# Performance work log

Measured on AMD Instinct MI355X. Metric: run time of the kernel, lower is better.

The kernel has to match this reference:

```python
import jax, jax.numpy as jnp
import numpy as np

SEQ, B, D_IN, D_TRAJ, D_LSTM = 640, 40, 8, 32, 64
NH, DH = 4, 48  # n_head, att_out
EMB = NH * DH  # 192


def setup_inputs() -> dict:
    key = jax.random.key(0)
    ks = jax.random.split(key, 16)
    g = lambda k, shape: (jax.random.normal(k, shape, dtype=jnp.float32) * 0.05)
    z = lambda n: jnp.zeros((n,), jnp.float32)
    return {
        "hist": jax.random.normal(ks[0], (128, 5, 40, D_IN), dtype=jnp.float32),
        "adj": jnp.zeros((B, B), dtype=jnp.int32),  # unused (use_spatial=False)
        "W1": g(ks[1], (D_TRAJ, D_IN)), "b1": z(D_TRAJ),
        "W_ih": g(ks[2], (4 * D_LSTM, D_TRAJ)), "W_hh": g(ks[3], (4 * D_LSTM, D_LSTM)),
        "b_ih": z(4 * D_LSTM), "b_hh": z(4 * D_LSTM),
        "Wq": g(ks[4], (EMB, D_LSTM)), "bq": z(EMB),
        "Wk": g(ks[5], (EMB, D_LSTM)), "bk": z(EMB),
        "Wv": g(ks[6], (EMB, D_LSTM)), "bv": z(EMB),
        "Wa": g(ks[7], (D_LSTM, EMB)), "ba": z(D_LSTM),
        "Wg": g(ks[8], (D_LSTM, EMB)), "bg": z(D_LSTM),
        "gamma": jnp.ones((D_LSTM,), jnp.float32), "beta": z(D_LSTM),
    }


def reference(hist, adj, W1, b1, W_ih, W_hh, b_ih, b_hh,
              Wq, bq, Wk, bk, Wv, bv, Wa, ba, Wg, bg, gamma, beta):
    # trajectory embedding + ELU
    x = jax.nn.elu(jnp.einsum('...f,hf->...h', hist, W1) + b1)
    x = x.reshape(SEQ, B, D_TRAJ)  # hardcoded (128*5, 40, 32) in the module

    # single-layer LSTM (torch gate order i, f, g, o), seq-first
    def step(carry, xt):
        h, c = carry
        gates = xt @ W_ih.T + h @ W_hh.T + b_ih + b_hh
        i, f, g_, o = jnp.split(gates, 4, axis=-1)
        c = jax.nn.sigmoid(f) * c + jax.nn.sigmoid(i) * jnp.tanh(g_)
        h = jax.nn.sigmoid(o) * jnp.tanh(c)
        return (h, c), h

    h0 = jnp.zeros((B, D_LSTM), x.dtype)
    (_, _), seq = jax.lax.scan(step, (h0, h0), x)  # (640, 40, 64)

    # multi-head attention over the 40-agent axis, per time step
    def heads(W, b):
        y = seq @ W.T + b  # (640, 40, 192)
        return y.reshape(SEQ, B, NH, DH).transpose(2, 0, 1, 3)  # (4, 640, 40, 48)

    q, k, v = heads(Wq, bq), heads(Wk, bk), heads(Wv, bv)
    a = jax.nn.softmax(jnp.einsum('hnqd,hnkd->hnqk', q, k) / 8.0, axis=-1)  # /sqrt(64)
    o = jnp.einsum('hnqk,hnkd->hnqd', a, v)  # (4, 640, 40, 48)
    o = o.transpose(1, 2, 0, 3).reshape(SEQ, B, EMB)  # recombine heads -> (640, 40, 192)

    # GLU (dropout rate = 0)
    tv = (o @ Wa.T + ba) * jax.nn.sigmoid(o @ Wg.T + bg)  # (640, 40, 64)

    # Add & LayerNorm (residual with LSTM output)
    y = seq + tv
    mu = y.mean(-1, keepdims=True)
    var = ((y - mu) ** 2).mean(-1, keepdims=True)
    return (y - mu) / jnp.sqrt(var + 1e-5) * gamma + beta
```

## Files before the change

### kernel.cpp

```cpp
#include <hip/hip_runtime.h>

#define SEQ 640
#define BATCH 40
#define D_IN 8
#define D_TRAJ 32
#define D_LSTM 64
#define G4 256
#define NH 4
#define DH 48
#define EMB 192

typedef float v2f __attribute__((ext_vector_type(2)));
typedef float v4f __attribute__((ext_vector_type(4)));
typedef _Float16 h2t __attribute__((ext_vector_type(2)));

__device__ __forceinline__ float sigmoid_f(float x) {
    float e = __expf(-x);
    return __builtin_amdgcn_rcpf(1.f + e);
}
__device__ __forceinline__ float tanh_f(float x) {
    float e = __expf(2.f * x);
    return 1.f - 2.f * __builtin_amdgcn_rcpf(e + 1.f);
}

__global__ void __launch_bounds__(256) k_embed(
    const float* __restrict__ hist, const float* __restrict__ W1,
    const float* __restrict__ b1, const float* __restrict__ W_ih,
    const float* __restrict__ b_ih, const float* __restrict__ b_hh,
    float* __restrict__ gates_x)
{
    __shared__ float sh_hist[BATCH * D_IN];
    __shared__ __align__(16) float sh_traj[BATCH * D_TRAJ];
    const int t = blockIdx.x, tid = threadIdx.x;

    for (int i = tid; i < BATCH * D_IN; i += 256)
        sh_hist[i] = hist[t * BATCH * D_IN + i];
    __syncthreads();

    for (int idx = tid; idx < BATCH * D_TRAJ; idx += 256) {
        int b = idx >> 5, h = idx & 31;
        float acc = b1[h];
        #pragma unroll
        for (int f = 0; f < D_IN; ++f)
            acc += sh_hist[b * D_IN + f] * W1[h * D_IN + f];
        sh_traj[idx] = acc > 0.f ? acc : (__expf(acc) - 1.f);
    }
    __syncthreads();

    float w[D_TRAJ];
    {
        const v4f* wv = (const v4f*)(W_ih + tid * D_TRAJ);
        #pragma unroll
        for (int u = 0; u < 8; ++u) {
            v4f x = wv[u];
            w[4*u] = x.x; w[4*u+1] = x.y; w[4*u+2] = x.z; w[4*u+3] = x.w;
        }
    }
    const float bias = b_ih[tid] + b_hh[tid];
    const int j = tid & 63, g = tid >> 6;

    for (int b = 0; b < BATCH; ++b) {
        const v4f* tp = (const v4f*)&sh_traj[b * D_TRAJ];
        float acc = bias;
        #pragma unroll
        for (int u = 0; u < 8; ++u) {
            v4f tv = tp[u];
            acc += tv.x * w[4*u];
            acc += tv.y * w[4*u+1];
            acc += tv.z * w[4*u+2];
            acc += tv.w * w[4*u+3];
        }
        gates_x[(((size_t)b * 4 + g) * SEQ + t) * 64 + j] = acc;
    }
}

__global__ void __launch_bounds__(256, 1) k_lstm(
    const float* __restrict__ gates_x, const float* __restrict__ W_hh,
    float* __restrict__ seq_out)
{
    const int b = blockIdx.x;
    const int tid = threadIdx.x;
    const int g = tid >> 6;
    const int j = tid & 63;

    __shared__ float sg[2][4][64];

    h2t w2[32];
    {
        const float* Wrow = W_hh + (g * 64 + j) * D_LSTM;
        #pragma unroll
        for (int m = 0; m < 32; ++m)
            w2[m] = (h2t){(_Float16)Wrow[2*m], (_Float16)Wrow[2*m+1]};
    }

    const float* gx = gates_x + (((size_t)b * 4 + g) * SEQ) * 64 + j;
    float gq0 = gx[0 * 64];
    float gq1 = gx[1 * 64];
    float gq2 = gx[2 * 64];
    float gq3 = gx[3 * 64];

    float h = 0.f, c = 0.f;
    float hpf = 0.f;
    const bool odd = (j & 1);

    auto step = [&](float& gq, int t) {
        const int hbits = __builtin_bit_cast(int, hpf);

        float a0 = gq, a1 = 0.f, a2 = 0.f, a3 = 0.f;
        #pragma unroll
        for (int m = 0; m < 8; ++m) {
            h2t p = __builtin_bit_cast(h2t, __builtin_amdgcn_readlane(hbits, 2*m));
            a0 = __builtin_amdgcn_fdot2(w2[m], p, a0, false);
        }
        #pragma unroll
        for (int m = 8; m < 16; ++m) {
            h2t p = __builtin_bit_cast(h2t, __builtin_amdgcn_readlane(hbits, 2*m));
            a1 = __builtin_amdgcn_fdot2(w2[m], p, a1, false);
        }
        #pragma unroll
        for (int m = 16; m < 24; ++m) {
            h2t p = __builtin_bit_cast(h2t, __builtin_amdgcn_readlane(hbits, 2*m));
            a2 = __builtin_amdgcn_fdot2(w2[m], p, a2, false);
        }
        #pragma unroll
        for (int m = 24; m < 32; ++m) {
            h2t p = __builtin_bit_cast(h2t, __builtin_amdgcn_readlane(hbits, 2*m));
            a3 = __builtin_amdgcn_fdot2(w2[m], p, a3, false);
        }
        float a = (a0 + a1) + (a2 + a3);

        const int buf = t & 1;
        sg[buf][g][j] = a;
        __syncthreads();
        float ai = sg[buf][0][j];
        float af = sg[buf][1][j];
        float ag = sg[buf][2][j];
        float ao = sg[buf][3][j];

        c = sigmoid_f(af) * c + sigmoid_f(ai) * tanh_f(ag);
        h = sigmoid_f(ao) * tanh_f(c);
        if (g == 0)
            seq_out[(size_t)(t * BATCH + b) * D_LSTM + j] = h;

        int own = (int)__builtin_bit_cast(unsigned short, (_Float16)h);
        int nb  = __builtin_amdgcn_update_dpp(0, own, 0xB1, 0xF, 0xF, true);
        int pk  = odd ? (nb | (own << 16)) : (own | (nb << 16));
        hpf = __builtin_bit_cast(float, pk);

        int tp = t + 4; if (tp > SEQ - 1) tp = SEQ - 1;
        gq = gx[(size_t)tp * 64];
    };

    for (int t = 0; t < SEQ; t += 4) {
        step(gq0, t + 0);
        step(gq1, t + 1);
        step(gq2, t + 2);
        step(gq3, t + 3);
    }
}

#define SAS 68
#define SKVS 152
#define SSS 44
__global__ void __launch_bounds__(256) k_attn(
    const float* __restrict__ seq,
    const float* __restrict__ Wq, const float* __restrict__ bq,
    const float* __restrict__ Wk, const float* __restrict__ bk,
    const float* __restrict__ Wv, const float* __restrict__ bv,
    float* __restrict__ o_buf)
{
    const int h = blockIdx.x, t = blockIdx.y, tid = threadIdx.x;
    __shared__ float sA[BATCH * SAS];
    __shared__ _Float16 skqv[BATCH * SKVS];
    __shared__ float ss[BATCH * SSS];

    for (int i = tid; i < BATCH * D_LSTM; i += 256)
        sA[(i >> 6) * SAS + (i & 63)] = seq[(size_t)t * BATCH * D_LSTM + i];
    __syncthreads();

    if (tid < 144) {
        int m = tid / 48, d = tid - m * 48;
        const float* W = (m == 0) ? Wq : (m == 1) ? Wk : Wv;
        const float* B = (m == 0) ? bq : (m == 1) ? bk : bv;
        const float* wrow = W + (h * DH + d) * D_LSTM;
        float wreg[D_LSTM];
        {
            const v4f* wv = (const v4f*)wrow;
            #pragma unroll
            for (int u = 0; u < 16; ++u) {
                v4f x = wv[u];
                wreg[4*u] = x.x; wreg[4*u+1] = x.y;
                wreg[4*u+2] = x.z; wreg[4*u+3] = x.w;
            }
        }
        const float bias = B[h * DH + d];

        for (int a = 0; a < BATCH; ++a) {
            const v4f* ap = (const v4f*)&sA[a * SAS];
            float acc = bias;
            #pragma unroll
            for (int u = 0; u < 16; ++u) {
                v4f av = ap[u];
                acc += av.x * wreg[4*u]   + av.y * wreg[4*u+1]
                     + av.z * wreg[4*u+2] + av.w * wreg[4*u+3];
            }
            skqv[a * SKVS + tid] = (_Float16)acc;
        }
    }
    __syncthreads();

    for (int idx = tid; idx < BATCH * BATCH; idx += 256) {
        int i = idx / BATCH, jj = idx % BATCH;
        const v4f* qp = (const v4f*)&skqv[i * SKVS];
        const v4f* kp = (const v4f*)&skqv[jj * SKVS + 48];
        float acc = 0.f;
        #pragma unroll
        for (int u = 0; u < 6; ++u) {
            v4f qv = qp[u], kv = kp[u];
            acc = __builtin_amdgcn_fdot2(__builtin_bit_cast(h2t, qv.x),
                    __builtin_bit_cast(h2t, kv.x), acc, false);
            acc = __builtin_amdgcn_fdot2(__builtin_bit_cast(h2t, qv.y),
                    __builtin_bit_cast(h2t, kv.y), acc, false);
            acc = __builtin_amdgcn_fdot2(__builtin_bit_cast(h2t, qv.z),
                    __builtin_bit_cast(h2t, kv.z), acc, false);
            acc = __builtin_amdgcn_fdot2(__builtin_bit_cast(h2t, qv.w),
                    __builtin_bit_cast(h2t, kv.w), acc, false);
        }
        ss[i * SSS + jj] = acc * 0.125f;
    }
    __syncthreads();

    if (tid < BATCH) {
        v4f* rp = (v4f*)&ss[tid * SSS];
        v4f r[10];
        #pragma unroll
        for (int u = 0; u < 10; ++u) r[u] = rp[u];
        float m = -1e30f;
        #pragma unroll
        for (int u = 0; u < 10; ++u)
            m = fmaxf(m, fmaxf(fmaxf(r[u].x, r[u].y), fmaxf(r[u].z, r[u].w)));
        float s = 0.f;
        #pragma unroll
        for (int u = 0; u < 10; ++u) {
            r[u].x = __expf(r[u].x - m); s += r[u].x;
            r[u].y = __expf(r[u].y - m); s += r[u].y;
            r[u].z = __expf(r[u].z - m); s += r[u].z;
            r[u].w = __expf(r[u].w - m); s += r[u].w;
        }
        float inv = __builtin_amdgcn_rcpf(s);
        #pragma unroll
        for (int u = 0; u < 10; ++u) {
            r[u].x *= inv; r[u].y *= inv; r[u].z *= inv; r[u].w *= inv;
            rp[u] = r[u];
        }
    }
    __syncthreads();

    if (tid < 240) {
        int bi = tid / 6, dg = tid % 6, d0 = dg * 8;
        const v4f* sp = (const v4f*)&ss[bi * SSS];
        v4f sr[10];
        #pragma unroll
        for (int u = 0; u < 10; ++u) sr[u] = sp[u];
        float acc[8];
        #pragma unroll
        for (int d = 0; d < 8; ++d) acc[d] = 0.f;
        for (int jj = 0; jj < 40; ++jj) {
            float a = ((const float*)&sr[jj >> 2])[jj & 3];
            v4f vv = *(const v4f*)&skqv[jj * SKVS + 96 + d0];
            #pragma unroll
            for (int w = 0; w < 4; ++w) {
                h2t pr = __builtin_bit_cast(h2t, ((const float*)&vv)[w]);
                acc[2 * w]     += a * (float)pr[0];
                acc[2 * w + 1] += a * (float)pr[1];
            }
        }
        float* ob = &o_buf[((size_t)t * BATCH + bi) * EMB + h * DH + d0];
        *(v4f*)&ob[0] = (v4f){acc[0], acc[1], acc[2], acc[3]};
        *(v4f*)&ob[4] = (v4f){acc[4], acc[5], acc[6], acc[7]};
    }
}

__global__ void __launch_bounds__(256) k_glu_ln(
    const float* __restrict__ seq, const float* __restrict__ obuf,
    const float* __restrict__ Wa, const float* __restrict__ ba,
    const float* __restrict__ Wg, const float* __restrict__ bg,
    const float* __restrict__ gamma, const float* __restrict__ beta,
    float* __restrict__ out)
{
    const int t = blockIdx.x, tid = threadIdx.x;
    __shared__ __align__(16) float so[BATCH * 196];
    __shared__ float sy[BATCH * 65];
    __shared__ float sseq[BATCH * D_LSTM];

    const float* ot = obuf + (size_t)t * BATCH * EMB;
    for (int i = tid; i < BATCH * EMB; i += 256)
        so[(i / EMB) * 196 + (i % EMB)] = ot[i];
    for (int i = tid; i < BATCH * D_LSTM; i += 256)
        sseq[i] = seq[(size_t)t * BATCH * D_LSTM + i];
    __syncthreads();

    const int j = tid >> 2, bgr = tid & 3;
    float acc_a[10], acc_g[10];
    #pragma unroll
    for (int bb = 0; bb < 10; ++bb) { acc_a[bb] = ba[j]; acc_g[bb] = bg[j]; }

    const v4f* wav = (const v4f*)(Wa + j * EMB);
    const v4f* wgv = (const v4f*)(Wg + j * EMB);
    for (int p4 = 0; p4 < EMB / 4; ++p4) {
        v4f av = wav[p4], gv = wgv[p4];
        #pragma unroll
        for (int bb = 0; bb < 10; ++bb) {
            v4f ov = *(const v4f*)&so[(bgr + 4 * bb) * 196 + 4 * p4];
            acc_a[bb] += ov.x * av.x;
            acc_a[bb] += ov.y * av.y;
            acc_a[bb] += ov.z * av.z;
            acc_a[bb] += ov.w * av.w;
            acc_g[bb] += ov.x * gv.x;
            acc_g[bb] += ov.y * gv.y;
            acc_g[bb] += ov.z * gv.z;
            acc_g[bb] += ov.w * gv.w;
        }
    }
    #pragma unroll
    for (int bb = 0; bb < 10; ++bb) {
        int b = bgr + 4 * bb;
        float tv = acc_a[bb] * sigmoid_f(acc_g[bb]);
        sy[b * 65 + j] = sseq[b * D_LSTM + j] + tv;
    }
    __syncthreads();

    const int w = tid >> 6, lane = tid & 63;
    const float gm = gamma[lane], bt = beta[lane];
    for (int rr = 0; rr < 10; ++rr) {
        int b = w + 4 * rr;
        float y = sy[b * 65 + lane];
        float s1 = y, s2 = y * y;
        #pragma unroll
        for (int m = 1; m < 64; m <<= 1) {
            s1 += __shfl_xor(s1, m, 64);
            s2 += __shfl_xor(s2, m, 64);
        }
        float mu  = s1 * (1.f / 64.f);
        float var = s2 * (1.f / 64.f) - mu * mu;
        float inv = rsqrtf(var + 1e-5f);
        out[(size_t)t * BATCH * D_LSTM + b * D_LSTM + lane] =
            (y - mu) * inv * gm + bt;
    }
}

extern "C" void kernel_launch(void* const* d_in, const int* in_sizes, int n_in,
                              void* d_out, int out_size, void* d_ws, size_t ws_size,
                              hipStream_t stream)
{
    const float* hist = (const float*)d_in[0];
    const float* W1   = (const float*)d_in[2];
    const float* b1   = (const float*)d_in[3];
    const float* W_ih = (const float*)d_in[4];
    const float* W_hh = (const float*)d_in[5];
    const float* b_ih = (const float*)d_in[6];
    const float* b_hh = (const float*)d_in[7];
    const float* Wq   = (const float*)d_in[8];
    const float* bq   = (const float*)d_in[9];
    const float* Wk   = (const float*)d_in[10];
    const float* bk   = (const float*)d_in[11];
    const float* Wv   = (const float*)d_in[12];
    const float* bv   = (const float*)d_in[13];
    const float* Wa   = (const float*)d_in[14];
    const float* ba   = (const float*)d_in[15];
    const float* Wg   = (const float*)d_in[16];
    const float* bg   = (const float*)d_in[17];
    const float* gamma = (const float*)d_in[18];
    const float* beta  = (const float*)d_in[19];
    float* out = (float*)d_out;

    float* ws = (float*)d_ws;
    float* gates_x = ws;
    float* seq     = ws + 6553600;
    float* obuf    = ws + 6553600 + 1638400;

    hipLaunchKernelGGL(k_embed, dim3(SEQ), dim3(256), 0, stream,
                       hist, W1, b1, W_ih, b_ih, b_hh, gates_x);
    hipLaunchKernelGGL(k_lstm, dim3(BATCH), dim3(256), 0, stream,
                       gates_x, W_hh, seq);
    hipLaunchKernelGGL(k_attn, dim3(NH, SEQ), dim3(256), 0, stream,
                       seq, Wq, bq, Wk, bk, Wv, bv, obuf);
    hipLaunchKernelGGL(k_glu_ln, dim3(SEQ), dim3(256), 0, stream,
                       seq, obuf, Wa, ba, Wg, bg, gamma, beta, out);
}
```

Baseline: 458.7 us.

## Split LSTM recurrent matvec by K-slices across waves with gate-interleaved layout

Each wave now computes partial sums for all four gates of its hidden unit over a 16-element slice of h, instead of one gate over the full 64-element h. The partials are reduced through shared memory with vector loads. The precomputed input gates are re-laid out so that the i,f,g,o values for one unit are contiguous and load as a single v4f. This shortens the serial fdot2 chain per step and cuts the number of readlanes per wave. In exchange, every wave computes the nonlinearities redundantly and reads more from shared memory per step.

```diff
diff --git a/kernel.cpp b/kernel.cpp
--- a/kernel.cpp
+++ b/kernel.cpp
@@ -70,7 +70,7 @@
             acc += tv.z * w[4*u+2];
             acc += tv.w * w[4*u+3];
         }
-        gates_x[(((size_t)b * 4 + g) * SEQ + t) * 64 + j] = acc;
+        gates_x[((size_t)b * SEQ + t) * G4 + j * 4 + g] = acc;
     }
 }
 
@@ -80,66 +80,64 @@
 {
     const int b = blockIdx.x;
     const int tid = threadIdx.x;
-    const int g = tid >> 6;
+    const int w = tid >> 6;
     const int j = tid & 63;
 
-    __shared__ float sg[2][4][64];
-
-    h2t w2[32];
-    {
-        const float* Wrow = W_hh + (g * 64 + j) * D_LSTM;
-        #pragma unroll
-        for (int m = 0; m < 32; ++m)
-            w2[m] = (h2t){(_Float16)Wrow[2*m], (_Float16)Wrow[2*m+1]};
-    }
-
-    const float* gx = gates_x + (((size_t)b * 4 + g) * SEQ) * 64 + j;
-    float gq0 = gx[0 * 64];
-    float gq1 = gx[1 * 64];
-    float gq2 = gx[2 * 64];
-    float gq3 = gx[3 * 64];
+    __shared__ __align__(16) float sg[2][4][64][4];
+
+    h2t wk[4][8];
+    #pragma unroll
+    for (int gg = 0; gg < 4; ++gg) {
+        const float* Wrow = W_hh + (gg * 64 + j) * D_LSTM + 16 * w;
+        #pragma unroll
+        for (int k = 0; k < 8; ++k)
+            wk[gg][k] = (h2t){(_Float16)Wrow[2*k], (_Float16)Wrow[2*k+1]};
+    }
+
+    const v4f* gxp = (const v4f*)(gates_x + (size_t)b * SEQ * G4) + j;
+    v4f gq0 = (v4f){0.f, 0.f, 0.f, 0.f};
+    v4f gq1 = gq0, gq2 = gq0, gq3 = gq0;
+    if (w == 0) {
+        gq0 = gxp[0 * 64];
+        gq1 = gxp[1 * 64];
+        gq2 = gxp[2 * 64];
+        gq3 = gxp[3 * 64];
+    }
 
     float h = 0.f, c = 0.f;
     float hpf = 0.f;
     const bool odd = (j & 1);
-
-    auto step = [&](float& gq, int t) {
+    const int lbase = 16 * w;
+
+    auto step = [&](v4f& gq, int t) {
         const int hbits = __builtin_bit_cast(int, hpf);
 
-        float a0 = gq, a1 = 0.f, a2 = 0.f, a3 = 0.f;
-        #pragma unroll
-        for (int m = 0; m < 8; ++m) {
-            h2t p = __builtin_bit_cast(h2t, __builtin_amdgcn_readlane(hbits, 2*m));
-            a0 = __builtin_amdgcn_fdot2(w2[m], p, a0, false);
-        }
-        #pragma unroll
-        for (int m = 8; m < 16; ++m) {
-            h2t p = __builtin_bit_cast(h2t, __builtin_amdgcn_readlane(hbits, 2*m));
-            a1 = __builtin_amdgcn_fdot2(w2[m], p, a1, false);
-        }
-        #pragma unroll
-        for (int m = 16; m < 24; ++m) {
-            h2t p = __builtin_bit_cast(h2t, __builtin_amdgcn_readlane(hbits, 2*m));
-            a2 = __builtin_amdgcn_fdot2(w2[m], p, a2, false);
-        }
-        #pragma unroll
-        for (int m = 24; m < 32; ++m) {
-            h2t p = __builtin_bit_cast(h2t, __builtin_amdgcn_readlane(hbits, 2*m));
-            a3 = __builtin_amdgcn_fdot2(w2[m], p, a3, false);
-        }
-        float a = (a0 + a1) + (a2 + a3);
+        float pi = gq.x, pf = gq.y, pg = gq.z, po = gq.w;
+        #pragma unroll
+        for (int k = 0; k < 8; ++k) {
+            h2t p = __builtin_bit_cast(h2t,
+                        __builtin_amdgcn_readlane(hbits, lbase + 2 * k));
+            pi = __builtin_amdgcn_fdot2(wk[0][k], p, pi, false);
+            pf = __builtin_amdgcn_fdot2(wk[1][k], p, pf, false);
+            pg = __builtin_amdgcn_fdot2(wk[2][k], p, pg, false);
+            po = __builtin_amdgcn_fdot2(wk[3][k], p, po, false);
+        }
 
         const int buf = t & 1;
-        sg[buf][g][j] = a;
+        *(v4f*)&sg[buf][w][j][0] = (v4f){pi, pf, pg, po};
         __syncthreads();
-        float ai = sg[buf][0][j];
-        float af = sg[buf][1][j];
-        float ag = sg[buf][2][j];
-        float ao = sg[buf][3][j];
+        v4f p0 = *(const v4f*)&sg[buf][0][j][0];
+        v4f p1 = *(const v4f*)&sg[buf][1][j][0];
+        v4f p2 = *(const v4f*)&sg[buf][2][j][0];
+        v4f p3 = *(const v4f*)&sg[buf][3][j][0];
+        float ai = (p0.x + p1.x) + (p2.x + p3.x);
+        float af = (p0.y + p1.y) + (p2.y + p3.y);
+        float ag = (p0.z + p1.z) + (p2.z + p3.z);
+        float ao = (p0.w + p1.w) + (p2.w + p3.w);
 
         c = sigmoid_f(af) * c + sigmoid_f(ai) * tanh_f(ag);
         h = sigmoid_f(ao) * tanh_f(c);
-        if (g == 0)
+        if (w == 0)
             seq_out[(size_t)(t * BATCH + b) * D_LSTM + j] = h;
 
         int own = (int)__builtin_bit_cast(unsigned short, (_Float16)h);
@@ -147,8 +145,10 @@
         int pk  = odd ? (nb | (own << 16)) : (own | (nb << 16));
         hpf = __builtin_bit_cast(float, pk);
 
-        int tp = t + 4; if (tp > SEQ - 1) tp = SEQ - 1;
-        gq = gx[(size_t)tp * 64];
+        if (w == 0) {
+            int tp = t + 4; if (tp > SEQ - 1) tp = SEQ - 1;
+            gq = gxp[(size_t)tp * 64];
+        }
     };
 
     for (int t = 0; t < SEQ; t += 4) {
```

Result: slower. 572.3 us (+24.8%).
